# Kernel tuning notes

Measured on AMD Instinct MI355X. Metric: run time of the kernel, lower is better.

Reference implementation:

```python
import jax, jax.numpy as jnp
import numpy as np

BETA = 0.25  # commitment_beta


def setup_inputs() -> dict:
    key = jax.random.key(0)
    k1, k2 = jax.random.split(key)
    B, S, D, K = 4, 2048, 256, 8192
    z_e = jax.random.normal(k1, (B, S, D), dtype=jnp.float32)
    # codebook init ~ uniform(-1/K, 1/K) in the original; scale is irrelevant for correctness,
    # use normal scaled similarly small.
    codebook = jax.random.uniform(k2, (K, D), dtype=jnp.float32, minval=-1.0 / K, maxval=1.0 / K)
    return {"z_e": z_e, "codebook": codebook}


def reference(z_e, codebook):
    B, S, D = z_e.shape
    flat = z_e.reshape(-1, D)  # [N, D], N = B*S
    distances = (
        jnp.sum(flat * flat, axis=1, keepdims=True)
        - 2.0 * (flat @ codebook.T)
        + jnp.sum(codebook * codebook, axis=1)[None, :]
    )
    indices = jnp.argmin(distances, axis=1)  # [N]
    z_q = codebook[indices].reshape(B, S, D)
    codebook_loss = jnp.mean((jax.lax.stop_gradient(z_e) - z_q) ** 2)
    commitment_loss = jnp.mean((z_e - jax.lax.stop_gradient(z_q)) ** 2)
    vq_loss = codebook_loss + BETA * commitment_loss
    # straight-through estimator
    z_q_st = z_e + jax.lax.stop_gradient(z_q - z_e)
    return z_q_st, indices.reshape(B, S), vq_loss
```

## Files before the change

kernel.cpp:

```cpp
#include <hip/hip_runtime.h>
#include <stdint.h>

#define N_ROWS  8192
#define DIM     256
#define K_CODES 8192
#define SPLITK  8
#define KS      1024
#define NT      128
#define LSLOTS  16
#define GSLOTS  12
#define MARGIN_ACC 1.0e-4f

typedef unsigned long long u64;
typedef unsigned short u16;
typedef short s16x8 __attribute__((ext_vector_type(8)));
typedef float f32x4 __attribute__((ext_vector_type(4)));

__device__ __forceinline__ u64 u64min(u64 a, u64 b) { return a < b ? a : b; }

__device__ __forceinline__ u16 f2bf(float f) {
    unsigned u = __float_as_uint(f);
    u += 0x7fffu + ((u >> 16) & 1u);
    return (u16)(u >> 16);
}

__device__ __forceinline__ void gld16(void* lds, const void* g) {
    __builtin_amdgcn_global_load_lds(
        (const __attribute__((address_space(1))) unsigned int*)g,
        (__attribute__((address_space(3))) unsigned int*)lds, 16, 0, 0);
}

__global__ __launch_bounds__(256) void vq_prep(const float* __restrict__ z_e,
                                               const float* __restrict__ cb,
                                               u16* __restrict__ zb,
                                               u16* __restrict__ cbb,
                                               float* __restrict__ xnorm,
                                               float* __restrict__ cnorm) {
    int wid  = (blockIdx.x * 256 + threadIdx.x) >> 6;
    int lane = threadIdx.x & 63;
    const float* src; u16* d16; float* dn;
    if (wid < N_ROWS) { src = z_e + (size_t)wid * DIM; d16 = zb + (size_t)wid * DIM; dn = xnorm + wid; }
    else              { int k = wid - N_ROWS;
                        src = cb  + (size_t)k   * DIM; d16 = cbb + (size_t)k * DIM; dn = cnorm + k; }
    float4 v = *(const float4*)(src + lane * 4);
    ushort4 h;
    h.x = f2bf(v.x); h.y = f2bf(v.y); h.z = f2bf(v.z); h.w = f2bf(v.w);
    *(ushort4*)(d16 + lane * 4) = h;
    float s = (v.x * v.x + v.y * v.y) + (v.z * v.z + v.w * v.w);
#pragma unroll
    for (int off = 1; off < 64; off <<= 1)
        s += __shfl_xor(s, off, 64);
    if (lane == 0) *dn = s;
}

__global__ __launch_bounds__(256, 2) void vq_mfma(const u16* __restrict__ zb,
                                                  const u16* __restrict__ cbb,
                                                  int* __restrict__ cand_cnt,
                                                  int* __restrict__ cand_idx) {
    __shared__ u16   Cs[3][128 * 64];
    __shared__ float lcd[128 * LSLOTS];
    __shared__ int   lci[128 * LSLOTS];
    __shared__ int   lcnt[128];
    __shared__ float gmaxs[128];

    const int tid   = threadIdx.x;
    const int lane  = tid & 63;
    const int wave  = tid >> 6;
    const int quad  = lane >> 4;
    const int l16   = lane & 15;
    const int split = blockIdx.x;
    const int n0    = blockIdx.y * 128;

    if (tid < 128) lcnt[tid] = 0;

    const int srow8  = lane >> 3;
    const int schunk = lane & 7;
    const int ssw    = (schunk ^ srow8) * 8;
    const u16* csrc  = cbb + (size_t)split * KS * DIM + (size_t)srow8 * DIM + ssw;

    s16x8 af[2][8];
#pragma unroll
    for (int i = 0; i < 2; i++) {
        const u16* p = zb + (size_t)(n0 + wave * 32 + i * 16 + l16) * DIM + quad * 8;
#pragma unroll
        for (int s = 0; s < 8; s++)
            af[i][s] = *(const s16x8*)(p + s * 32);
    }

    auto STAGE = [&](int s, int bw) {
        const u16* src = csrc + (size_t)(s >> 2) * (NT * DIM) + (s & 3) * 64;
#pragma unroll
        for (int t = 0; t < 4; t++) {
            int rg = wave * 4 + t;
            gld16(&Cs[bw][rg * 512], src + (size_t)rg * (8 * DIM));
        }
    };

    float runmax[8];
#pragma unroll
    for (int t = 0; t < 8; t++) runmax[t] = -3.0e38f;

    STAGE(0, 0);
    STAGE(1, 1);
    asm volatile("s_waitcnt vmcnt(4)" ::: "memory");
    __builtin_amdgcn_s_barrier();

    int bufR = 0, bufW = 2;

    for (int kt = 0; kt < 8; kt++) {
        const int kbase = split * KS + kt * NT;
        f32x4 acc[2][8];
#pragma unroll
        for (int i = 0; i < 2; i++)
#pragma unroll
            for (int j = 0; j < 8; j++)
#pragma unroll
                for (int e = 0; e < 4; e++) acc[i][j][e] = 0.0f;

#pragma unroll
        for (int kc = 0; kc < 4; kc++) {
            const int it = (kt << 2) | kc;
            if (it < 30) STAGE(it + 2, bufW);

            const u16* cbuf = &Cs[bufR][0];
#pragma unroll
            for (int ks = 0; ks < 2; ks++) {
                s16x8 bfr[8];
#pragma unroll
                for (int j = 0; j < 8; j++)
                    bfr[j] = *(const s16x8*)&cbuf[(j * 16 + l16) * 64 +
                                                  (((ks << 2) | quad) ^ (l16 & 7)) * 8];
#pragma unroll
                for (int i = 0; i < 2; i++)
#pragma unroll
                    for (int j = 0; j < 8; j++)
                        acc[i][j] = __builtin_amdgcn_mfma_f32_16x16x32_bf16(
                            af[i][kc * 2 + ks], bfr[j], acc[i][j], 0, 0, 0);
            }

            if (it < 30) {
                asm volatile("s_waitcnt vmcnt(4)" ::: "memory");
                __builtin_amdgcn_s_barrier();
            } else if (it == 30) {
                asm volatile("s_waitcnt vmcnt(0)" ::: "memory");
                __builtin_amdgcn_s_barrier();
            }
            bufR = bufR == 2 ? 0 : bufR + 1;
            bufW = bufW == 2 ? 0 : bufW + 1;
        }

#pragma unroll
        for (int i = 0; i < 2; i++)
#pragma unroll
            for (int r = 0; r < 4; r++) {
                float m = fmaxf(fmaxf(fmaxf(acc[i][0][r], acc[i][1][r]),
                                      fmaxf(acc[i][2][r], acc[i][3][r])),
                                fmaxf(fmaxf(acc[i][4][r], acc[i][5][r]),
                                      fmaxf(acc[i][6][r], acc[i][7][r])));
                m = fmaxf(m, __shfl_xor(m, 1, 64));
                m = fmaxf(m, __shfl_xor(m, 2, 64));
                m = fmaxf(m, __shfl_xor(m, 4, 64));
                m = fmaxf(m, __shfl_xor(m, 8, 64));
                runmax[i * 4 + r] = fmaxf(runmax[i * 4 + r], m);
                float thr = runmax[i * 4 + r] - MARGIN_ACC;
                int rl = wave * 32 + i * 16 + quad * 4 + r;
#pragma unroll
                for (int j = 0; j < 8; j++) {
                    float d = acc[i][j][r];
                    if (d >= thr) {
                        int pos = atomicAdd(&lcnt[rl], 1);
                        if (pos < LSLOTS) {
                            lcd[rl * LSLOTS + pos] = d;
                            lci[rl * LSLOTS + pos] = kbase + j * 16 + l16;
                        }
                    }
                }
            }
    }

    if (l16 == 0) {
#pragma unroll
        for (int i = 0; i < 2; i++)
#pragma unroll
            for (int r = 0; r < 4; r++)
                gmaxs[wave * 32 + i * 16 + quad * 4 + r] = runmax[i * 4 + r];
    }
    __syncthreads();

    if (tid < 128) {
        int n   = n0 + tid;
        int cnt = lcnt[tid]; if (cnt > LSLOTS) cnt = LSLOTS;
        float thrf = gmaxs[tid] - MARGIN_ACC;
        int base = (n * SPLITK + split) * GSLOTS;
        int w = 0;
        for (int s = 0; s < cnt && w < GSLOTS; s++)
            if (lcd[tid * LSLOTS + s] >= thrf)
                cand_idx[base + w++] = lci[tid * LSLOTS + s];
        cand_cnt[n * SPLITK + split] = w;
    }
}

__global__ __launch_bounds__(256) void vq_finalize(const float* __restrict__ z_e,
                                                   const float* __restrict__ cb,
                                                   const float* __restrict__ xnorm,
                                                   const float* __restrict__ cnorm,
                                                   const int* __restrict__ cand_cnt,
                                                   const int* __restrict__ cand_idx,
                                                   float* __restrict__ out_zq,
                                                   float* __restrict__ out_idx,
                                                   float* __restrict__ rowloss) {
    const int n    = blockIdx.x * 4 + (threadIdx.x >> 6);
    const int lane = threadIdx.x & 63;

    int myidx = -1;
    int t = 0;
#pragma unroll
    for (int s = 0; s < SPLITK; s++) {
        int c = cand_cnt[n * SPLITK + s];
        if (lane >= t && lane < t + c)
            myidx = cand_idx[(n * SPLITK + s) * GSLOTS + (lane - t)];
        t += c;
    }

    u64 key = ~0ULL;
    if (myidx >= 0) {
        const float* xr = z_e + (size_t)n * DIM;
        const float* cr = cb + (size_t)myidx * DIM;
        float acc = 0.0f;
#pragma unroll 8
        for (int d = 0; d < DIM; d++)
            acc = __builtin_fmaf(xr[d], cr[d], acc);
        float dist = __builtin_fmaf(-2.0f, acc, xnorm[n]) + cnorm[myidx];
        key = ((u64)__float_as_uint(dist) << 32) | (unsigned)myidx;
    }
#pragma unroll
    for (int off = 1; off < 64; off <<= 1)
        key = u64min(key, __shfl_xor(key, off, 64));

    int idx = (int)(unsigned)(key & 0xffffffffu);
    if (key == ~0ULL) idx = 0;

    float4 x = *(const float4*)(z_e + (size_t)n * DIM + lane * 4);
    float4 c = *(const float4*)(cb + (size_t)idx * DIM + lane * 4);
    float4 st;
    st.x = x.x + (c.x - x.x); st.y = x.y + (c.y - x.y);
    st.z = x.z + (c.z - x.z); st.w = x.w + (c.w - x.w);
    *(float4*)(out_zq + (size_t)n * DIM + lane * 4) = st;

    float d0 = x.x - c.x, d1 = x.y - c.y, d2 = x.z - c.z, d3 = x.w - c.w;
    float s2 = (d0 * d0 + d1 * d1) + (d2 * d2 + d3 * d3);
#pragma unroll
    for (int off = 1; off < 64; off <<= 1)
        s2 += __shfl_xor(s2, off, 64);
    if (lane == 0) {
        rowloss[n] = s2;
        out_idx[n] = (float)idx;
    }
}

__global__ __launch_bounds__(256) void vq_loss(const float* __restrict__ rowloss,
                                               float* __restrict__ out_loss) {
    __shared__ double sd[256];
    double s = 0.0;
    for (int i = threadIdx.x; i < N_ROWS; i += 256) s += (double)rowloss[i];
    sd[threadIdx.x] = s;
    __syncthreads();
    for (int off = 128; off; off >>= 1) {
        if (threadIdx.x < off) sd[threadIdx.x] += sd[threadIdx.x + off];
        __syncthreads();
    }
    if (threadIdx.x == 0) {
        double mean = sd[0] / (double)((size_t)N_ROWS * DIM);
        out_loss[0] = (float)(1.25 * mean);
    }
}

extern "C" void kernel_launch(void* const* d_in, const int* in_sizes, int n_in,
                              void* d_out, int out_size, void* d_ws, size_t ws_size,
                              hipStream_t stream) {
    const float* z_e = (const float*)d_in[0];
    const float* cb  = (const float*)d_in[1];

    float* out   = (float*)d_out;
    float* zq    = out;
    float* oidx  = out + (size_t)N_ROWS * DIM;
    float* oloss = oidx + N_ROWS;

    u16*   zb       = (u16*)d_ws;
    u16*   cbb      = zb + (size_t)N_ROWS * DIM;
    float* xnorm    = (float*)(cbb + (size_t)K_CODES * DIM);
    float* cnorm    = xnorm + N_ROWS;
    float* rowloss  = cnorm + K_CODES;
    int*   cand_cnt = (int*)(rowloss + N_ROWS);
    int*   cand_idx = cand_cnt + N_ROWS * SPLITK;

    vq_prep    <<<(N_ROWS + K_CODES) / 4, 256, 0, stream>>>(z_e, cb, zb, cbb, xnorm, cnorm);
    vq_mfma    <<<dim3(SPLITK, N_ROWS / 128), 256, 0, stream>>>(zb, cbb, cand_cnt, cand_idx);
    vq_finalize<<<N_ROWS / 4, 256, 0, stream>>>(z_e, cb, xnorm, cnorm, cand_cnt, cand_idx, zq, oidx, rowloss);
    vq_loss    <<<1, 256, 0, stream>>>(rowloss, oloss);
}
```

Baseline: 180.5 us.

## Double the codebook split and pipeline smaller stages through a four-slot LDS ring

Doubles the split-K factor so each block scans 512 codes instead of 1024, which doubles the grid and shrinks the global candidate slots. The codebook staging is reorganized into 64x64 sub-tiles over a 4-slot LDS ring with a 3-deep prefetch, and the barrier now comes before each stage issue. Each phase issues half as many MFMAs per barrier. This aims to raise occupancy and parallelism and to hide load latency better, at the cost of more barriers, more candidate-merge work per row, and fewer candidate slots per split.

```diff
diff --git a/kernel.cpp b/kernel.cpp
--- a/kernel.cpp
+++ b/kernel.cpp
@@ -4,11 +4,11 @@
 #define N_ROWS  8192
 #define DIM     256
 #define K_CODES 8192
-#define SPLITK  8
-#define KS      1024
+#define SPLITK  16
+#define KS      512
 #define NT      128
 #define LSLOTS  16
-#define GSLOTS  12
+#define GSLOTS  8
 #define MARGIN_ACC 1.0e-4f
 
 typedef unsigned long long u64;
@@ -28,6 +28,12 @@
     __builtin_amdgcn_global_load_lds(
         (const __attribute__((address_space(1))) unsigned int*)g,
         (__attribute__((address_space(3))) unsigned int*)lds, 16, 0, 0);
+}
+
+__device__ __forceinline__ void block_barrier() {
+    asm volatile("" ::: "memory");
+    __builtin_amdgcn_s_barrier();
+    asm volatile("" ::: "memory");
 }
 
 __global__ __launch_bounds__(256) void vq_prep(const float* __restrict__ z_e,
@@ -57,7 +63,7 @@
                                                   const u16* __restrict__ cbb,
                                                   int* __restrict__ cand_cnt,
                                                   int* __restrict__ cand_idx) {
-    __shared__ u16   Cs[3][128 * 64];
+    __shared__ u16   Cs[4][64 * 64];
     __shared__ float lcd[128 * LSLOTS];
     __shared__ int   lci[128 * LSLOTS];
     __shared__ int   lcnt[128];
@@ -87,68 +93,40 @@
             af[i][s] = *(const s16x8*)(p + s * 32);
     }
 
-    auto STAGE = [&](int s, int bw) {
-        const u16* src = csrc + (size_t)(s >> 2) * (NT * DIM) + (s & 3) * 64;
-#pragma unroll
-        for (int t = 0; t < 4; t++) {
-            int rg = wave * 4 + t;
-            gld16(&Cs[bw][rg * 512], src + (size_t)rg * (8 * DIM));
+    auto STAGE = [&](int s, int slot) {
+        const int kts = s >> 3, pls = s & 7;
+        const u16* src = csrc + (size_t)(kts * NT + (pls & 1) * 64) * DIM + (pls >> 1) * 64;
+#pragma unroll
+        for (int t = 0; t < 2; t++) {
+            int rg = wave * 2 + t;
+            gld16(&Cs[slot][rg * 512], src + (size_t)rg * (8 * DIM));
         }
     };
 
+    f32x4 acc[2][8];
     float runmax[8];
 #pragma unroll
     for (int t = 0; t < 8; t++) runmax[t] = -3.0e38f;
 
-    STAGE(0, 0);
-    STAGE(1, 1);
-    asm volatile("s_waitcnt vmcnt(4)" ::: "memory");
-    __builtin_amdgcn_s_barrier();
-
-    int bufR = 0, bufW = 2;
-
-    for (int kt = 0; kt < 8; kt++) {
-        const int kbase = split * KS + kt * NT;
-        f32x4 acc[2][8];
-#pragma unroll
-        for (int i = 0; i < 2; i++)
-#pragma unroll
-            for (int j = 0; j < 8; j++)
-#pragma unroll
-                for (int e = 0; e < 4; e++) acc[i][j][e] = 0.0f;
-
-#pragma unroll
-        for (int kc = 0; kc < 4; kc++) {
-            const int it = (kt << 2) | kc;
-            if (it < 30) STAGE(it + 2, bufW);
-
-            const u16* cbuf = &Cs[bufR][0];
-#pragma unroll
-            for (int ks = 0; ks < 2; ks++) {
-                s16x8 bfr[8];
-#pragma unroll
-                for (int j = 0; j < 8; j++)
-                    bfr[j] = *(const s16x8*)&cbuf[(j * 16 + l16) * 64 +
-                                                  (((ks << 2) | quad) ^ (l16 & 7)) * 8];
-#pragma unroll
-                for (int i = 0; i < 2; i++)
-#pragma unroll
-                    for (int j = 0; j < 8; j++)
-                        acc[i][j] = __builtin_amdgcn_mfma_f32_16x16x32_bf16(
-                            af[i][kc * 2 + ks], bfr[j], acc[i][j], 0, 0, 0);
-            }
-
-            if (it < 30) {
-                asm volatile("s_waitcnt vmcnt(4)" ::: "memory");
-                __builtin_amdgcn_s_barrier();
-            } else if (it == 30) {
-                asm volatile("s_waitcnt vmcnt(0)" ::: "memory");
-                __builtin_amdgcn_s_barrier();
-            }
-            bufR = bufR == 2 ? 0 : bufR + 1;
-            bufW = bufW == 2 ? 0 : bufW + 1;
+    auto PHASE = [&](int pl) {
+        const u16* cbuf = &Cs[pl & 3][0];
+#pragma unroll
+        for (int ks = 0; ks < 2; ks++) {
+            s16x8 bfr[4];
+#pragma unroll
+            for (int jj = 0; jj < 4; jj++)
+                bfr[jj] = *(const s16x8*)&cbuf[(jj * 16 + l16) * 64 +
+                                               (((ks << 2) | quad) ^ (l16 & 7)) * 8];
+#pragma unroll
+            for (int i = 0; i < 2; i++)
+#pragma unroll
+                for (int jj = 0; jj < 4; jj++)
+                    acc[i][(pl & 1) * 4 + jj] = __builtin_amdgcn_mfma_f32_16x16x32_bf16(
+                        af[i][(pl >> 1) * 2 + ks], bfr[jj], acc[i][(pl & 1) * 4 + jj], 0, 0, 0);
         }
-
+    };
+
+    auto EPILOGUE = [&](int kbase) {
 #pragma unroll
         for (int i = 0; i < 2; i++)
 #pragma unroll
@@ -176,6 +154,52 @@
                     }
                 }
             }
+    };
+
+    STAGE(0, 0); STAGE(1, 1); STAGE(2, 2);
+
+    for (int kt = 0; kt < 3; kt++) {
+        const int kbase = split * KS + kt * NT;
+#pragma unroll
+        for (int i = 0; i < 2; i++)
+#pragma unroll
+            for (int j = 0; j < 8; j++)
+#pragma unroll
+                for (int e = 0; e < 4; e++) acc[i][j][e] = 0.0f;
+#pragma unroll
+        for (int pl = 0; pl < 8; pl++) {
+            asm volatile("s_waitcnt vmcnt(4) lgkmcnt(0)" ::: "memory");
+            block_barrier();
+            STAGE(kt * 8 + pl + 3, (pl + 3) & 3);
+            PHASE(pl);
+        }
+        EPILOGUE(kbase);
+    }
+    {
+        const int kbase = split * KS + 3 * NT;
+#pragma unroll
+        for (int i = 0; i < 2; i++)
+#pragma unroll
+            for (int j = 0; j < 8; j++)
+#pragma unroll
+                for (int e = 0; e < 4; e++) acc[i][j][e] = 0.0f;
+#pragma unroll
+        for (int pl = 0; pl < 5; pl++) {
+            asm volatile("s_waitcnt vmcnt(4) lgkmcnt(0)" ::: "memory");
+            block_barrier();
+            STAGE(24 + pl + 3, (pl + 3) & 3);
+            PHASE(pl);
+        }
+        asm volatile("s_waitcnt vmcnt(4) lgkmcnt(0)" ::: "memory");
+        block_barrier();
+        PHASE(5);
+        asm volatile("s_waitcnt vmcnt(2) lgkmcnt(0)" ::: "memory");
+        block_barrier();
+        PHASE(6);
+        asm volatile("s_waitcnt vmcnt(0) lgkmcnt(0)" ::: "memory");
+        block_barrier();
+        PHASE(7);
+        EPILOGUE(kbase);
     }
 
     if (l16 == 0) {
```

After: 196.8 us. +9.0%, slower.

## Keep top candidates with bf16 dots and prune across splits before exact rescoring

Applied to the files above, without the earlier changes.

The MFMA kernel now keeps the best GSLOTS candidates by approximate dot product instead of the first ones that pass the threshold, and writes those dot values out. It also moves the candidate arrays to a split-major layout. The finalize kernel takes a max of the approximate dots across all splits and runs the exact fp32 rescoring only for candidates within the margin. This cuts the number of 256-length fp32 dot products per row. Barriers now also wait on lgkmcnt, which adds some synchronisation cost.

```diff
diff --git a/kernel.cpp b/kernel.cpp
--- a/kernel.cpp
+++ b/kernel.cpp
@@ -8,7 +8,7 @@
 #define KS      1024
 #define NT      128
 #define LSLOTS  16
-#define GSLOTS  12
+#define GSLOTS  8
 #define MARGIN_ACC 1.0e-4f
 
 typedef unsigned long long u64;
@@ -28,6 +28,12 @@
     __builtin_amdgcn_global_load_lds(
         (const __attribute__((address_space(1))) unsigned int*)g,
         (__attribute__((address_space(3))) unsigned int*)lds, 16, 0, 0);
+}
+
+__device__ __forceinline__ void block_barrier() {
+    asm volatile("" ::: "memory");
+    __builtin_amdgcn_s_barrier();
+    asm volatile("" ::: "memory");
 }
 
 __global__ __launch_bounds__(256) void vq_prep(const float* __restrict__ z_e,
@@ -56,7 +62,8 @@
 __global__ __launch_bounds__(256, 2) void vq_mfma(const u16* __restrict__ zb,
                                                   const u16* __restrict__ cbb,
                                                   int* __restrict__ cand_cnt,
-                                                  int* __restrict__ cand_idx) {
+                                                  int* __restrict__ cand_idx,
+                                                  float* __restrict__ cand_dot) {
     __shared__ u16   Cs[3][128 * 64];
     __shared__ float lcd[128 * LSLOTS];
     __shared__ int   lci[128 * LSLOTS];
@@ -102,8 +109,8 @@
 
     STAGE(0, 0);
     STAGE(1, 1);
-    asm volatile("s_waitcnt vmcnt(4)" ::: "memory");
-    __builtin_amdgcn_s_barrier();
+    asm volatile("s_waitcnt vmcnt(4) lgkmcnt(0)" ::: "memory");
+    block_barrier();
 
     int bufR = 0, bufW = 2;
 
@@ -139,11 +146,11 @@
             }
 
             if (it < 30) {
-                asm volatile("s_waitcnt vmcnt(4)" ::: "memory");
-                __builtin_amdgcn_s_barrier();
+                asm volatile("s_waitcnt vmcnt(4) lgkmcnt(0)" ::: "memory");
+                block_barrier();
             } else if (it == 30) {
-                asm volatile("s_waitcnt vmcnt(0)" ::: "memory");
-                __builtin_amdgcn_s_barrier();
+                asm volatile("s_waitcnt vmcnt(0) lgkmcnt(0)" ::: "memory");
+                block_barrier();
             }
             bufR = bufR == 2 ? 0 : bufR + 1;
             bufW = bufW == 2 ? 0 : bufW + 1;
@@ -191,12 +198,25 @@
         int n   = n0 + tid;
         int cnt = lcnt[tid]; if (cnt > LSLOTS) cnt = LSLOTS;
         float thrf = gmaxs[tid] - MARGIN_ACC;
-        int base = (n * SPLITK + split) * GSLOTS;
+        float bd[GSLOTS]; int bi[GSLOTS];
         int w = 0;
-        for (int s = 0; s < cnt && w < GSLOTS; s++)
-            if (lcd[tid * LSLOTS + s] >= thrf)
-                cand_idx[base + w++] = lci[tid * LSLOTS + s];
-        cand_cnt[n * SPLITK + split] = w;
+        for (int s = 0; s < cnt; s++) {
+            float d = lcd[tid * LSLOTS + s];
+            if (d < thrf) continue;
+            if (w < GSLOTS) { bd[w] = d; bi[w] = lci[tid * LSLOTS + s]; w++; }
+            else {
+                int mn = 0;
+#pragma unroll
+                for (int k = 1; k < GSLOTS; k++) if (bd[k] < bd[mn]) mn = k;
+                if (d > bd[mn]) { bd[mn] = d; bi[mn] = lci[tid * LSLOTS + s]; }
+            }
+        }
+        int base = (split * N_ROWS + n) * GSLOTS;
+        for (int k = 0; k < w; k++) {
+            cand_idx[base + k] = bi[k];
+            cand_dot[base + k] = bd[k];
+        }
+        cand_cnt[split * N_ROWS + n] = w;
     }
 }
 
@@ -206,24 +226,33 @@
                                                    const float* __restrict__ cnorm,
                                                    const int* __restrict__ cand_cnt,
                                                    const int* __restrict__ cand_idx,
+                                                   const float* __restrict__ cand_dot,
                                                    float* __restrict__ out_zq,
                                                    float* __restrict__ out_idx,
                                                    float* __restrict__ rowloss) {
     const int n    = blockIdx.x * 4 + (threadIdx.x >> 6);
     const int lane = threadIdx.x & 63;
 
-    int myidx = -1;
+    int   myidx = -1;
+    float mydot = -3.0e38f;
     int t = 0;
 #pragma unroll
     for (int s = 0; s < SPLITK; s++) {
-        int c = cand_cnt[n * SPLITK + s];
-        if (lane >= t && lane < t + c)
-            myidx = cand_idx[(n * SPLITK + s) * GSLOTS + (lane - t)];
+        int c = cand_cnt[s * N_ROWS + n];
+        if (lane >= t && lane < t + c) {
+            myidx = cand_idx[(s * N_ROWS + n) * GSLOTS + (lane - t)];
+            mydot = cand_dot[(s * N_ROWS + n) * GSLOTS + (lane - t)];
+        }
         t += c;
     }
 
+    float mg = mydot;
+#pragma unroll
+    for (int off = 1; off < 64; off <<= 1)
+        mg = fmaxf(mg, __shfl_xor(mg, off, 64));
+
     u64 key = ~0ULL;
-    if (myidx >= 0) {
+    if (myidx >= 0 && mydot >= mg - MARGIN_ACC) {
         const float* xr = z_e + (size_t)n * DIM;
         const float* cr = cb + (size_t)myidx * DIM;
         float acc = 0.0f;
@@ -293,9 +322,10 @@
     float* rowloss  = cnorm + K_CODES;
     int*   cand_cnt = (int*)(rowloss + N_ROWS);
     int*   cand_idx = cand_cnt + N_ROWS * SPLITK;
+    float* cand_dot = (float*)(cand_idx + (size_t)N_ROWS * SPLITK * GSLOTS);
 
     vq_prep    <<<(N_ROWS + K_CODES) / 4, 256, 0, stream>>>(z_e, cb, zb, cbb, xnorm, cnorm);
-    vq_mfma    <<<dim3(SPLITK, N_ROWS / 128), 256, 0, stream>>>(zb, cbb, cand_cnt, cand_idx);
-    vq_finalize<<<N_ROWS / 4, 256, 0, stream>>>(z_e, cb, xnorm, cnorm, cand_cnt, cand_idx, zq, oidx, rowloss);
+    vq_mfma    <<<dim3(SPLITK, N_ROWS / 128), 256, 0, stream>>>(zb, cbb, cand_cnt, cand_idx, cand_dot);
+    vq_finalize<<<N_ROWS / 4, 256, 0, stream>>>(z_e, cb, xnorm, cnorm, cand_cnt, cand_idx, cand_dot, zq, oidx, rowloss);
     vq_loss    <<<1, 256, 0, stream>>>(rowloss, oloss);
 }
```

Measured after the change: 175.6 us. 2.7% less time.
